# Kernel optimization log

Measured on AMD Instinct MI355X. Metric: run time of the kernel, lower is better.

The kernel has to match this reference:

```python
import jax, jax.numpy as jnp
import numpy as np

TEMP1 = 4.0  # local_temp1 default


def setup_inputs() -> dict:
    key = jax.random.key(0)
    k1, k2 = jax.random.split(key)
    query = jax.random.normal(k1, (256, 768, 96), dtype=jnp.float32)
    context = jax.random.normal(k2, (256, 768, 19, 19), dtype=jnp.float32)
    return {"query": query, "context": context}


def reference(query, context):
    # query: [B, ndf, Q]; context: [B, ndf, ih, iw]
    B, ndf, Q = query.shape
    ih, iw = context.shape[2], context.shape[3]
    S = ih * iw
    ctx = context.reshape(B, ndf, S)            # [B, ndf, S]
    # attn = contextT @ query -> [B, S, Q]
    attn = jnp.einsum('bds,bdq->bsq', ctx, query)
    # softmax over query dim
    attn = jax.nn.softmax(attn, axis=-1)
    # transpose to [B, Q, S], temperature scale, softmax over source dim
    attn = jnp.swapaxes(attn, 1, 2) * TEMP1
    attn = jax.nn.softmax(attn, axis=-1)        # [B, Q, S]
    # weightedContext = context @ attn^T -> [B, ndf, Q]
    weighted_context = jnp.einsum('bds,bqs->bdq', ctx, attn)
    attn_map = attn.reshape(B, Q, ih, iw)
    return weighted_context, attn_map
```

## Files before the change

### kernel.cpp

```cpp
#include <hip/hip_runtime.h>

#define NB 256
#define NDF 768
#define NQ 96
#define NS 361
#define LDT 40
#define LDP 392
#define WSROW 368
#define CSROW 368
#define WS_LOG_BYTES ((size_t)NB * NQ * WSROW * 2)
#define WS_CTX_BYTES ((size_t)NB * NDF * CSROW * 2)
#define WS_FULL_BYTES (WS_LOG_BYTES + WS_CTX_BYTES)

typedef short bf16x8_t __attribute__((ext_vector_type(8)));
typedef float f32x4_t __attribute__((ext_vector_type(4)));
typedef float f32x4u_t __attribute__((ext_vector_type(4), aligned(4)));
typedef float f32x2u_t __attribute__((ext_vector_type(2), aligned(4)));
typedef unsigned int u32x2_t __attribute__((ext_vector_type(2)));
typedef unsigned int u32x4_t __attribute__((ext_vector_type(4)));

__device__ __forceinline__ unsigned pack_hi(unsigned b_, unsigned a_) {
    return __builtin_amdgcn_perm(b_, a_, 0x07060302u);
}
__device__ __forceinline__ unsigned short f2bf(float x) {
    unsigned u = __float_as_uint(x);
    u += 0x7FFFu + ((u >> 16) & 1u);
    return (unsigned short)(u >> 16);
}
__device__ __forceinline__ float bf2f(unsigned short h) {
    return __uint_as_float(((unsigned)h) << 16);
}

__device__ __forceinline__ void block_sync_lds() {
    __builtin_amdgcn_sched_barrier(0);
    asm volatile("s_waitcnt lgkmcnt(0)" ::: "memory");
    __builtin_amdgcn_sched_barrier(0);
    __builtin_amdgcn_s_barrier();
    __builtin_amdgcn_sched_barrier(0);
}

template<int MODE>
__global__ __launch_bounds__(384, 3) void k1_gemm1_softmaxq(
    const float* __restrict__ Qg, const float* __restrict__ Cg,
    unsigned short* __restrict__ WsLog, unsigned* __restrict__ WsCtxD,
    float* __restrict__ AoutF)
{
    __shared__ unsigned short sQhi[NQ * LDT];
    __shared__ unsigned short sQlo[NQ * LDT];
    __shared__ unsigned short sShi[192 * LDT];
    __shared__ unsigned short sSlo[192 * LDT];

    const int b = blockIdx.x >> 1;
    const int h = blockIdx.x & 1;
    const int tid = threadIdx.x;
    const int wv = tid >> 6;
    const int lane = tid & 63;
    const int ll = lane & 15;
    const int lg = lane >> 4;
    const int s0 = 192 * h;
    const int qq  = tid % NQ;
    const int kqQ = tid / NQ;
    const int sp  = tid % 96;
    const int kqb = tid / 96;
    const int sA0 = s0 + 2 * sp;
    const bool ok0 = (sA0 < NS);
    const bool ok1 = (sA0 + 1 < NS);
    const int wsCol = 96 * h + sp;
    const bool wok = (MODE == 2) && (wsCol < 184);

    const float* __restrict__ qg = Qg + (size_t)b * NDF * NQ;
    const float* __restrict__ cg = Cg + (size_t)b * NDF * NS;
    unsigned* __restrict__ wscd = (MODE == 2) ? (WsCtxD + (size_t)b * NDF * 184) : nullptr;

    f32x4_t acc[6][2];
#pragma unroll
    for (int i = 0; i < 6; ++i)
#pragma unroll
        for (int j = 0; j < 2; ++j) acc[i][j] = (f32x4_t)0.0f;

    float RQa[8], RQb[8];
    float RCa[16], RCb[16];

#define LOADQ(K0, R) { \
    const float* p = qg + ((K0) + 4 * kqQ) * NQ + qq; \
    R[0] = p[0]; R[1] = p[NQ]; R[2] = p[2 * NQ]; R[3] = p[3 * NQ]; \
    const float* p2 = p + 16 * NQ; \
    R[4] = p2[0]; R[5] = p2[NQ]; R[6] = p2[2 * NQ]; R[7] = p2[3 * NQ]; }

#define LOADC(K0, R) { \
    _Pragma("unroll") \
    for (int k2 = 0; k2 < 2; ++k2) { \
        const float* p = cg + ((K0) + 4 * (kqb + 4 * k2)) * NS; \
        _Pragma("unroll") \
        for (int j = 0; j < 4; ++j) { \
            const float* pj = p + j * NS + sA0; \
            f32x2u_t v; \
            if (ok1) { v = *(const f32x2u_t*)pj; } \
            else { v[0] = ok0 ? pj[0] : 0.0f; v[1] = 0.0f; } \
            R[(k2 * 4 + j) * 2 + 0] = v[0]; \
            R[(k2 * 4 + j) * 2 + 1] = v[1]; } } }

#define STOREQ(R) { \
    _Pragma("unroll") \
    for (int t = 0; t < 2; ++t) { \
        unsigned u0 = __float_as_uint(R[4*t+0]), u1 = __float_as_uint(R[4*t+1]); \
        unsigned u2 = __float_as_uint(R[4*t+2]), u3 = __float_as_uint(R[4*t+3]); \
        float l0 = R[4*t+0] - __uint_as_float(u0 & 0xFFFF0000u); \
        float l1 = R[4*t+1] - __uint_as_float(u1 & 0xFFFF0000u); \
        float l2 = R[4*t+2] - __uint_as_float(u2 & 0xFFFF0000u); \
        float l3 = R[4*t+3] - __uint_as_float(u3 & 0xFFFF0000u); \
        u32x2_t hi, lo; \
        hi[0] = pack_hi(u1, u0); hi[1] = pack_hi(u3, u2); \
        lo[0] = pack_hi(__float_as_uint(l1), __float_as_uint(l0)); \
        lo[1] = pack_hi(__float_as_uint(l3), __float_as_uint(l2)); \
        int off = qq * LDT + 4 * (kqQ + 4 * t); \
        *(u32x2_t*)&sQhi[off] = hi; \
        *(u32x2_t*)&sQlo[off] = lo; } }

#define STOREC(K0, R) { \
    _Pragma("unroll") \
    for (int k2 = 0; k2 < 2; ++k2) { \
        const int kq = kqb + 4 * k2; \
        unsigned u[4][2]; float l[4][2]; \
        _Pragma("unroll") \
        for (int j = 0; j < 4; ++j) { \
            _Pragma("unroll") \
            for (int s1 = 0; s1 < 2; ++s1) { \
                float x = R[(k2 * 4 + j) * 2 + s1]; \
                u[j][s1] = __float_as_uint(x); \
                l[j][s1] = x - __uint_as_float(u[j][s1] & 0xFFFF0000u); } } \
        _Pragma("unroll") \
        for (int s1 = 0; s1 < 2; ++s1) { \
            u32x2_t hi, lo; \
            hi[0] = pack_hi(u[1][s1], u[0][s1]); \
            hi[1] = pack_hi(u[3][s1], u[2][s1]); \
            lo[0] = pack_hi(__float_as_uint(l[1][s1]), __float_as_uint(l[0][s1])); \
            lo[1] = pack_hi(__float_as_uint(l[3][s1]), __float_as_uint(l[2][s1])); \
            int off = (2 * sp + s1) * LDT + 4 * kq; \
            *(u32x2_t*)&sShi[off] = hi; \
            *(u32x2_t*)&sSlo[off] = lo; } \
        if (wok) { \
            _Pragma("unroll") \
            for (int j = 0; j < 4; ++j) \
                wscd[(size_t)((K0) + 4 * kq + j) * 184 + wsCol] = pack_hi(u[j][1], u[j][0]); } } }

#define FRAGMFMA() { \
    bf16x8_t Bhi[2], Blo[2]; \
    _Pragma("unroll") \
    for (int nt = 0; nt < 2; ++nt) { \
        int row = 32 * wv + 16 * nt + ll; \
        Bhi[nt] = *(const bf16x8_t*)&sShi[row * LDT + 8 * lg]; \
        Blo[nt] = *(const bf16x8_t*)&sSlo[row * LDT + 8 * lg]; } \
    _Pragma("unroll") \
    for (int mt = 0; mt < 6; ++mt) { \
        int row = 16 * mt + ll; \
        bf16x8_t Ahi = *(const bf16x8_t*)&sQhi[row * LDT + 8 * lg]; \
        bf16x8_t Alo = *(const bf16x8_t*)&sQlo[row * LDT + 8 * lg]; \
        _Pragma("unroll") \
        for (int nt = 0; nt < 2; ++nt) { \
            acc[mt][nt] = __builtin_amdgcn_mfma_f32_16x16x32_bf16(Ahi, Bhi[nt], acc[mt][nt], 0, 0, 0); \
            acc[mt][nt] = __builtin_amdgcn_mfma_f32_16x16x32_bf16(Ahi, Blo[nt], acc[mt][nt], 0, 0, 0); \
            acc[mt][nt] = __builtin_amdgcn_mfma_f32_16x16x32_bf16(Alo, Bhi[nt], acc[mt][nt], 0, 0, 0); } } }

    LOADQ(0, RQa); LOADC(0, RCa);
    for (int k0 = 0; k0 < NDF; k0 += 64) {
        STOREQ(RQa); STOREC(k0, RCa);
        block_sync_lds();
        if (k0 + 32 < NDF) { LOADQ(k0 + 32, RQb); LOADC(k0 + 32, RCb); }
        __builtin_amdgcn_sched_barrier(0);
        FRAGMFMA();
        block_sync_lds();
        STOREQ(RQb); STOREC(k0 + 32, RCb);
        block_sync_lds();
        if (k0 + 64 < NDF) { LOADQ(k0 + 64, RQa); LOADC(k0 + 64, RCa); }
        __builtin_amdgcn_sched_barrier(0);
        FRAGMFMA();
        block_sync_lds();
    }
#undef LOADQ
#undef LOADC
#undef STOREQ
#undef STOREC
#undef FRAGMFMA

#pragma unroll
    for (int nt = 0; nt < 2; ++nt) {
        float m = -3.0e38f;
#pragma unroll
        for (int mt = 0; mt < 6; ++mt)
#pragma unroll
            for (int r = 0; r < 4; ++r) m = fmaxf(m, acc[mt][nt][r]);
        m = fmaxf(m, __shfl_xor(m, 16));
        m = fmaxf(m, __shfl_xor(m, 32));
        float sum = 0.0f;
#pragma unroll
        for (int mt = 0; mt < 6; ++mt)
#pragma unroll
            for (int r = 0; r < 4; ++r) {
                float e = __expf(acc[mt][nt][r] - m);
                acc[mt][nt][r] = e;
                sum += e;
            }
        sum += __shfl_xor(sum, 16);
        sum += __shfl_xor(sum, 32);
        float inv = 4.0f / sum;
#pragma unroll
        for (int mt = 0; mt < 6; ++mt)
#pragma unroll
            for (int r = 0; r < 4; ++r) acc[mt][nt][r] *= inv;
    }

    if constexpr (MODE >= 1) {
        unsigned short* wr = WsLog + (size_t)b * NQ * WSROW;
#pragma unroll
        for (int mt = 0; mt < 6; ++mt)
#pragma unroll
            for (int nt = 0; nt < 2; ++nt)
#pragma unroll
                for (int r = 0; r < 4; ++r) {
                    int q = 16 * mt + 4 * lg + r;
                    int s = s0 + 32 * wv + 16 * nt + ll;
                    if (s < NS) wr[q * WSROW + s] = f2bf(acc[mt][nt][r]);
                }
    } else {
        float* aout = AoutF + (size_t)b * NQ * NS;
#pragma unroll
        for (int mt = 0; mt < 6; ++mt)
#pragma unroll
            for (int nt = 0; nt < 2; ++nt)
#pragma unroll
                for (int r = 0; r < 4; ++r) {
                    int q = 16 * mt + 4 * lg + r;
                    int s = s0 + 32 * wv + 16 * nt + ll;
                    if (s < NS) aout[(size_t)q * NS + s] = acc[mt][nt][r];
                }
    }
}

__global__ __launch_bounds__(256) void k15_softmaxs(float* __restrict__ Aout)
{
    const int b = blockIdx.x;
    const int q = blockIdx.y * 4 + (threadIdx.x >> 6);
    const int lane = threadIdx.x & 63;
    float* __restrict__ row = Aout + ((size_t)b * NQ + q) * NS;
    const int c0 = 6 * lane;

    float v[6];
#pragma unroll
    for (int i = 0; i < 6; ++i) v[i] = (c0 + i < NS) ? row[c0 + i] : -INFINITY;
    float m = v[0];
#pragma unroll
    for (int i = 1; i < 6; ++i) m = fmaxf(m, v[i]);
#pragma unroll
    for (int o = 1; o < 64; o <<= 1) m = fmaxf(m, __shfl_xor(m, o));
    float e[6], sum = 0.0f;
#pragma unroll
    for (int i = 0; i < 6; ++i) { e[i] = __expf(v[i] - m); sum += e[i]; }
#pragma unroll
    for (int o = 1; o < 64; o <<= 1) sum += __shfl_xor(sum, o);
    float inv = 1.0f / sum;
#pragma unroll
    for (int i = 0; i < 6; ++i) if (c0 + i < NS) row[c0 + i] = e[i] * inv;
}

template<int MODE>
__global__ __launch_bounds__(512, 4) void k2_gemm2(
    const float* __restrict__ Cg, const unsigned short* __restrict__ WsLog,
    const unsigned short* __restrict__ WsCtx,
    const float* __restrict__ AttnF, float* __restrict__ Wout, float* __restrict__ AoutF)
{
    extern __shared__ char smem2[];
    unsigned short* sP = (unsigned short*)smem2;
    unsigned* sPd = (unsigned*)smem2;
    float* sMax = (float*)(smem2 + NQ * LDP * 2);
    float* sInv = sMax + NQ;

    const int b = blockIdx.x >> 2;
    const int quarter = blockIdx.x & 3;
    const int tid = threadIdx.x;
    const int wv = tid >> 6;
    const int lane = tid & 63;
    const int ll = lane & 15;
    const int lg = lane >> 4;

    if constexpr (MODE >= 1) {
        const unsigned* __restrict__ wsd = (const unsigned*)(WsLog + (size_t)b * NQ * WSROW);
        for (int i = tid; i < NQ * 184; i += 512) {
            int r = i / 184, c = i - r * 184;
            sPd[r * 196 + c] = wsd[i];
        }
        for (int i = tid; i < NQ * 12; i += 512) {
            int r = i / 12, c = i - r * 12;
            sPd[r * 196 + 184 + c] = 0;
        }
        __syncthreads();

        const int l32 = tid & 31;
        const int rbase = tid >> 5;
#pragma unroll
        for (int pass = 0; pass < 6; ++pass) {
            int row = pass * 16 + rbase;
            float m = -3.0e38f;
#pragma unroll
            for (int j = 0; j < 6; ++j) {
                int dw = l32 + 32 * j;
                if (dw < 184) {
                    unsigned u = sPd[row * 196 + dw];
                    float v0 = bf2f((unsigned short)(u & 0xFFFFu));
                    float v1 = bf2f((unsigned short)(u >> 16));
                    if (2 * dw < NS) m = fmaxf(m, v0);
                    if (2 * dw + 1 < NS) m = fmaxf(m, v1);
                }
            }
#pragma unroll
            for (int o = 1; o < 32; o <<= 1) m = fmaxf(m, __shfl_xor(m, o));
            if (l32 == 0) sMax[row] = m;
        }
        __syncthreads();
#pragma unroll
        for (int pass = 0; pass < 6; ++pass) {
            int row = pass * 16 + rbase;
            float m = sMax[row];
            float sum = 0.0f;
#pragma unroll
            for (int j = 0; j < 6; ++j) {
                int dw = l32 + 32 * j;
                if (dw < 184) {
                    unsigned u = sPd[row * 196 + dw];
                    float v0 = bf2f((unsigned short)(u & 0xFFFFu));
                    float v1 = bf2f((unsigned short)(u >> 16));
                    float e0 = (2 * dw < NS) ? __expf(v0 - m) : 0.0f;
                    float e1 = (2 * dw + 1 < NS) ? __expf(v1 - m) : 0.0f;
                    sum += e0 + e1;
                    sPd[row * 196 + dw] = ((unsigned)f2bf(e1) << 16) | (unsigned)f2bf(e0);
                }
            }
#pragma unroll
            for (int o = 1; o < 32; o <<= 1) sum += __shfl_xor(sum, o);
            if (l32 == 0) sInv[row] = sum;
        }
        __syncthreads();
        if (tid < NQ) sInv[tid] = 1.0f / sInv[tid];
        __syncthreads();
        if (quarter == 0) {
            float* aout = AoutF + (size_t)b * NQ * NS;
            for (int i = tid; i < NQ * NS; i += 512) {
                int q = i / NS, s = i - q * NS;
                aout[i] = bf2f(sP[q * LDP + s]) * sInv[q];
            }
        }
    } else {
        const float* __restrict__ attn = AttnF + (size_t)b * NQ * NS;
        for (int i = tid; i < NQ * 181; i += 512) {
            int row = i / 181, p = i - row * 181;
            float x0 = attn[row * NS + 2 * p];
            float x1 = (p < 180) ? attn[row * NS + 2 * p + 1] : 0.0f;
            sPd[row * 196 + p] = pack_hi(__float_as_uint(x1), __float_as_uint(x0));
        }
        for (int i = tid; i < NQ * 15; i += 512) {
            int row = i / 15, p = i - row * 15;
            sPd[row * 196 + 181 + p] = 0;
        }
        __syncthreads();
    }

    f32x4_t acc[3][3];
#pragma unroll
    for (int i = 0; i < 3; ++i)
#pragma unroll
        for (int j = 0; j < 3; ++j) acc[i][j] = (f32x4_t)0.0f;

    const int dw = wv >> 1, qw = wv & 1;
    const float* __restrict__ cq = Cg + (size_t)b * NDF * NS + (size_t)(quarter * 192) * NS;
    const unsigned short* __restrict__ cb =
        (MODE == 2) ? (WsCtx + ((size_t)b * NDF + quarter * 192) * CSROW) : nullptr;

#pragma unroll
    for (int c = 0; c < 12; ++c) {
        bf16x8_t Bf[3];
#pragma unroll
        for (int nt = 0; nt < 3; ++nt) {
            int row = 16 * (3 * qw + nt) + ll;
            Bf[nt] = *(const bf16x8_t*)&sP[row * LDP + 32 * c + 8 * lg];
        }
#pragma unroll
        for (int i = 0; i < 3; ++i) {
            int d = 16 * (3 * dw + i) + ll;
            bf16x8_t Af;
            if constexpr (MODE == 2) {
                if (c < 11 || lg < 2) {
                    Af = *(const bf16x8_t*)&cb[(size_t)d * CSROW + 32 * c + 8 * lg];
                } else {
                    Af = (bf16x8_t)0;
                }
            } else {
                const float* ap = cq + (size_t)d * NS + 32 * c + 8 * lg;
                u32x4_t u;
                if (c < 11) {
                    f32x4u_t a0 = *(const f32x4u_t*)ap;
                    f32x4u_t a1 = *(const f32x4u_t*)(ap + 4);
                    u[0] = pack_hi(__float_as_uint(a0[1]), __float_as_uint(a0[0]));
                    u[1] = pack_hi(__float_as_uint(a0[3]), __float_as_uint(a0[2]));
                    u[2] = pack_hi(__float_as_uint(a1[1]), __float_as_uint(a1[0]));
                    u[3] = pack_hi(__float_as_uint(a1[3]), __float_as_uint(a1[2]));
                } else {
                    float t[8];
#pragma unroll
                    for (int e = 0; e < 8; ++e) {
                        int s = 352 + 8 * lg + e;
                        t[e] = (s < NS) ? ap[e] : 0.0f;
                    }
                    u[0] = pack_hi(__float_as_uint(t[1]), __float_as_uint(t[0]));
                    u[1] = pack_hi(__float_as_uint(t[3]), __float_as_uint(t[2]));
                    u[2] = pack_hi(__float_as_uint(t[5]), __float_as_uint(t[4]));
                    u[3] = pack_hi(__float_as_uint(t[7]), __float_as_uint(t[6]));
                }
                Af = __builtin_bit_cast(bf16x8_t, u);
            }
#pragma unroll
            for (int nt = 0; nt < 3; ++nt)
                acc[i][nt] = __builtin_amdgcn_mfma_f32_16x16x32_bf16(Af, Bf[nt], acc[i][nt], 0, 0, 0);
        }
    }

    float* wout = Wout + (size_t)b * NDF * NQ;
    float invq[3];
#pragma unroll
    for (int nt = 0; nt < 3; ++nt) {
        if constexpr (MODE >= 1) invq[nt] = sInv[16 * (3 * qw + nt) + ll];
        else invq[nt] = 1.0f;
    }
#pragma unroll
    for (int i = 0; i < 3; ++i)
#pragma unroll
        for (int nt = 0; nt < 3; ++nt)
#pragma unroll
            for (int r = 0; r < 4; ++r) {
                int d = quarter * 192 + 16 * (3 * dw + i) + 4 * lg + r;
                int q = 16 * (3 * qw + nt) + ll;
                wout[(size_t)d * NQ + q] = acc[i][nt][r] * invq[nt];
            }
}

extern "C" void kernel_launch(void* const* d_in, const int* in_sizes, int n_in,
                              void* d_out, int out_size, void* d_ws, size_t ws_size,
                              hipStream_t stream) {
    const float* Qg = (const float*)d_in[0];
    const float* Cg = (const float*)d_in[1];
    float* Wout = (float*)d_out;
    float* Aout = Wout + (size_t)NB * NDF * NQ;

    const int smem2 = NQ * LDP * 2 + NQ * 8;

    if (ws_size >= WS_FULL_BYTES) {
        unsigned short* wsLog = (unsigned short*)d_ws;
        unsigned* wsCtxD = (unsigned*)((char*)d_ws + WS_LOG_BYTES);
        k1_gemm1_softmaxq<2><<<dim3(NB * 2), dim3(384), 0, stream>>>(Qg, Cg, wsLog, wsCtxD, nullptr);
        (void)hipFuncSetAttribute((const void*)k2_gemm2<2>,
                                  hipFuncAttributeMaxDynamicSharedMemorySize, smem2);
        k2_gemm2<2><<<dim3(NB * 4), dim3(512), smem2, stream>>>(
            Cg, wsLog, (const unsigned short*)wsCtxD, nullptr, Wout, Aout);
    } else if (ws_size >= WS_LOG_BYTES) {
        unsigned short* wsLog = (unsigned short*)d_ws;
        k1_gemm1_softmaxq<1><<<dim3(NB * 2), dim3(384), 0, stream>>>(Qg, Cg, wsLog, nullptr, nullptr);
        (void)hipFuncSetAttribute((const void*)k2_gemm2<1>,
                                  hipFuncAttributeMaxDynamicSharedMemorySize, smem2);
        k2_gemm2<1><<<dim3(NB * 4), dim3(512), smem2, stream>>>(
            Cg, wsLog, nullptr, nullptr, Wout, Aout);
    } else {
        k1_gemm1_softmaxq<0><<<dim3(NB * 2), dim3(384), 0, stream>>>(Qg, Cg, nullptr, nullptr, Aout);
        k15_softmaxs<<<dim3(NB, 24), dim3(256), 0, stream>>>(Aout);
        (void)hipFuncSetAttribute((const void*)k2_gemm2<0>,
                                  hipFuncAttributeMaxDynamicSharedMemorySize, smem2);
        k2_gemm2<0><<<dim3(NB * 4), dim3(512), smem2, stream>>>(
            Cg, nullptr, nullptr, Aout, Wout, Aout);
    }
}
```

Measured before the change: 223.2 us.

## Split first GEMM into four source-column tiles per batch for higher occupancy

```diff
diff --git a/kernel.cpp b/kernel.cpp
--- a/kernel.cpp
+++ b/kernel.cpp
@@ -40,137 +40,101 @@
 }
 
 template<int MODE>
-__global__ __launch_bounds__(384, 3) void k1_gemm1_softmaxq(
+__global__ __launch_bounds__(384, 6) void k1_gemm1_softmaxq(
     const float* __restrict__ Qg, const float* __restrict__ Cg,
     unsigned short* __restrict__ WsLog, unsigned* __restrict__ WsCtxD,
     float* __restrict__ AoutF)
 {
     __shared__ unsigned short sQhi[NQ * LDT];
     __shared__ unsigned short sQlo[NQ * LDT];
-    __shared__ unsigned short sShi[192 * LDT];
-    __shared__ unsigned short sSlo[192 * LDT];
-
-    const int b = blockIdx.x >> 1;
-    const int h = blockIdx.x & 1;
+    __shared__ unsigned short sShi[NQ * LDT];
+    __shared__ unsigned short sSlo[NQ * LDT];
+
+    const int b = blockIdx.x >> 2;
+    const int h = blockIdx.x & 3;
     const int tid = threadIdx.x;
     const int wv = tid >> 6;
     const int lane = tid & 63;
     const int ll = lane & 15;
     const int lg = lane >> 4;
-    const int s0 = 192 * h;
-    const int qq  = tid % NQ;
-    const int kqQ = tid / NQ;
-    const int sp  = tid % 96;
-    const int kqb = tid / 96;
-    const int sA0 = s0 + 2 * sp;
+    const int s0 = 96 * h;
+    const int qp  = tid % 48;
+    const int kq8 = tid / 48;
+    const int sA0 = s0 + 2 * qp;
     const bool ok0 = (sA0 < NS);
     const bool ok1 = (sA0 + 1 < NS);
-    const int wsCol = 96 * h + sp;
+    const int wsCol = 48 * h + qp;
     const bool wok = (MODE == 2) && (wsCol < 184);
 
     const float* __restrict__ qg = Qg + (size_t)b * NDF * NQ;
     const float* __restrict__ cg = Cg + (size_t)b * NDF * NS;
     unsigned* __restrict__ wscd = (MODE == 2) ? (WsCtxD + (size_t)b * NDF * 184) : nullptr;
 
-    f32x4_t acc[6][2];
-#pragma unroll
-    for (int i = 0; i < 6; ++i)
-#pragma unroll
-        for (int j = 0; j < 2; ++j) acc[i][j] = (f32x4_t)0.0f;
-
-    float RQa[8], RQb[8];
-    float RCa[16], RCb[16];
+    f32x4_t acc[6];
+#pragma unroll
+    for (int i = 0; i < 6; ++i) acc[i] = (f32x4_t)0.0f;
+
+    float RQa[8], RQb[8], RCa[8], RCb[8];
 
 #define LOADQ(K0, R) { \
-    const float* p = qg + ((K0) + 4 * kqQ) * NQ + qq; \
-    R[0] = p[0]; R[1] = p[NQ]; R[2] = p[2 * NQ]; R[3] = p[3 * NQ]; \
-    const float* p2 = p + 16 * NQ; \
-    R[4] = p2[0]; R[5] = p2[NQ]; R[6] = p2[2 * NQ]; R[7] = p2[3 * NQ]; }
+    _Pragma("unroll") \
+    for (int j = 0; j < 4; ++j) { \
+        f32x2u_t v = *(const f32x2u_t*)(qg + ((K0) + 4 * kq8 + j) * NQ + 2 * qp); \
+        R[2*j+0] = v[0]; R[2*j+1] = v[1]; } }
 
 #define LOADC(K0, R) { \
     _Pragma("unroll") \
-    for (int k2 = 0; k2 < 2; ++k2) { \
-        const float* p = cg + ((K0) + 4 * (kqb + 4 * k2)) * NS; \
-        _Pragma("unroll") \
-        for (int j = 0; j < 4; ++j) { \
-            const float* pj = p + j * NS + sA0; \
-            f32x2u_t v; \
-            if (ok1) { v = *(const f32x2u_t*)pj; } \
-            else { v[0] = ok0 ? pj[0] : 0.0f; v[1] = 0.0f; } \
-            R[(k2 * 4 + j) * 2 + 0] = v[0]; \
-            R[(k2 * 4 + j) * 2 + 1] = v[1]; } } }
-
-#define STOREQ(R) { \
+    for (int j = 0; j < 4; ++j) { \
+        const float* pj = cg + ((K0) + 4 * kq8 + j) * NS + sA0; \
+        f32x2u_t v; \
+        if (ok1) { v = *(const f32x2u_t*)pj; } \
+        else { v[0] = ok0 ? pj[0] : 0.0f; v[1] = 0.0f; } \
+        R[2*j+0] = v[0]; R[2*j+1] = v[1]; } }
+
+#define STORE2(R, DSTH, DSTL) { \
     _Pragma("unroll") \
-    for (int t = 0; t < 2; ++t) { \
-        unsigned u0 = __float_as_uint(R[4*t+0]), u1 = __float_as_uint(R[4*t+1]); \
-        unsigned u2 = __float_as_uint(R[4*t+2]), u3 = __float_as_uint(R[4*t+3]); \
-        float l0 = R[4*t+0] - __uint_as_float(u0 & 0xFFFF0000u); \
-        float l1 = R[4*t+1] - __uint_as_float(u1 & 0xFFFF0000u); \
-        float l2 = R[4*t+2] - __uint_as_float(u2 & 0xFFFF0000u); \
-        float l3 = R[4*t+3] - __uint_as_float(u3 & 0xFFFF0000u); \
+    for (int s1 = 0; s1 < 2; ++s1) { \
+        unsigned u0 = __float_as_uint(R[0+s1]), u1 = __float_as_uint(R[2+s1]); \
+        unsigned u2 = __float_as_uint(R[4+s1]), u3 = __float_as_uint(R[6+s1]); \
+        float l0 = R[0+s1] - __uint_as_float(u0 & 0xFFFF0000u); \
+        float l1 = R[2+s1] - __uint_as_float(u1 & 0xFFFF0000u); \
+        float l2 = R[4+s1] - __uint_as_float(u2 & 0xFFFF0000u); \
+        float l3 = R[6+s1] - __uint_as_float(u3 & 0xFFFF0000u); \
         u32x2_t hi, lo; \
         hi[0] = pack_hi(u1, u0); hi[1] = pack_hi(u3, u2); \
         lo[0] = pack_hi(__float_as_uint(l1), __float_as_uint(l0)); \
         lo[1] = pack_hi(__float_as_uint(l3), __float_as_uint(l2)); \
-        int off = qq * LDT + 4 * (kqQ + 4 * t); \
-        *(u32x2_t*)&sQhi[off] = hi; \
-        *(u32x2_t*)&sQlo[off] = lo; } }
-
-#define STOREC(K0, R) { \
-    _Pragma("unroll") \
-    for (int k2 = 0; k2 < 2; ++k2) { \
-        const int kq = kqb + 4 * k2; \
-        unsigned u[4][2]; float l[4][2]; \
+        int off = (2 * qp + s1) * LDT + 4 * kq8; \
+        *(u32x2_t*)&(DSTH)[off] = hi; \
+        *(u32x2_t*)&(DSTL)[off] = lo; } }
+
+#define RELAYC(K0, R) { \
+    if (wok) { \
         _Pragma("unroll") \
-        for (int j = 0; j < 4; ++j) { \
-            _Pragma("unroll") \
-            for (int s1 = 0; s1 < 2; ++s1) { \
-                float x = R[(k2 * 4 + j) * 2 + s1]; \
-                u[j][s1] = __float_as_uint(x); \
-                l[j][s1] = x - __uint_as_float(u[j][s1] & 0xFFFF0000u); } } \
-        _Pragma("unroll") \
-        for (int s1 = 0; s1 < 2; ++s1) { \
-            u32x2_t hi, lo; \
-            hi[0] = pack_hi(u[1][s1], u[0][s1]); \
-            hi[1] = pack_hi(u[3][s1], u[2][s1]); \
-            lo[0] = pack_hi(__float_as_uint(l[1][s1]), __float_as_uint(l[0][s1])); \
-            lo[1] = pack_hi(__float_as_uint(l[3][s1]), __float_as_uint(l[2][s1])); \
-            int off = (2 * sp + s1) * LDT + 4 * kq; \
-            *(u32x2_t*)&sShi[off] = hi; \
-            *(u32x2_t*)&sSlo[off] = lo; } \
-        if (wok) { \
-            _Pragma("unroll") \
-            for (int j = 0; j < 4; ++j) \
-                wscd[(size_t)((K0) + 4 * kq + j) * 184 + wsCol] = pack_hi(u[j][1], u[j][0]); } } }
+        for (int j = 0; j < 4; ++j) \
+            wscd[(size_t)((K0) + 4 * kq8 + j) * 184 + wsCol] = \
+                pack_hi(__float_as_uint(R[2*j+1]), __float_as_uint(R[2*j+0])); } }
 
 #define FRAGMFMA() { \
-    bf16x8_t Bhi[2], Blo[2]; \
-    _Pragma("unroll") \
-    for (int nt = 0; nt < 2; ++nt) { \
-        int row = 32 * wv + 16 * nt + ll; \
-        Bhi[nt] = *(const bf16x8_t*)&sShi[row * LDT + 8 * lg]; \
-        Blo[nt] = *(const bf16x8_t*)&sSlo[row * LDT + 8 * lg]; } \
+    bf16x8_t Bhi = *(const bf16x8_t*)&sShi[(16 * wv + ll) * LDT + 8 * lg]; \
+    bf16x8_t Blo = *(const bf16x8_t*)&sSlo[(16 * wv + ll) * LDT + 8 * lg]; \
     _Pragma("unroll") \
     for (int mt = 0; mt < 6; ++mt) { \
-        int row = 16 * mt + ll; \
-        bf16x8_t Ahi = *(const bf16x8_t*)&sQhi[row * LDT + 8 * lg]; \
-        bf16x8_t Alo = *(const bf16x8_t*)&sQlo[row * LDT + 8 * lg]; \
-        _Pragma("unroll") \
-        for (int nt = 0; nt < 2; ++nt) { \
-            acc[mt][nt] = __builtin_amdgcn_mfma_f32_16x16x32_bf16(Ahi, Bhi[nt], acc[mt][nt], 0, 0, 0); \
-            acc[mt][nt] = __builtin_amdgcn_mfma_f32_16x16x32_bf16(Ahi, Blo[nt], acc[mt][nt], 0, 0, 0); \
-            acc[mt][nt] = __builtin_amdgcn_mfma_f32_16x16x32_bf16(Alo, Bhi[nt], acc[mt][nt], 0, 0, 0); } } }
+        bf16x8_t Ahi = *(const bf16x8_t*)&sQhi[(16 * mt + ll) * LDT + 8 * lg]; \
+        bf16x8_t Alo = *(const bf16x8_t*)&sQlo[(16 * mt + ll) * LDT + 8 * lg]; \
+        acc[mt] = __builtin_amdgcn_mfma_f32_16x16x32_bf16(Ahi, Bhi, acc[mt], 0, 0, 0); \
+        acc[mt] = __builtin_amdgcn_mfma_f32_16x16x32_bf16(Ahi, Blo, acc[mt], 0, 0, 0); \
+        acc[mt] = __builtin_amdgcn_mfma_f32_16x16x32_bf16(Alo, Bhi, acc[mt], 0, 0, 0); } }
 
     LOADQ(0, RQa); LOADC(0, RCa);
     for (int k0 = 0; k0 < NDF; k0 += 64) {
-        STOREQ(RQa); STOREC(k0, RCa);
+        STORE2(RQa, sQhi, sQlo); STORE2(RCa, sShi, sSlo); RELAYC(k0, RCa);
         block_sync_lds();
         if (k0 + 32 < NDF) { LOADQ(k0 + 32, RQb); LOADC(k0 + 32, RCb); }
         __builtin_amdgcn_sched_barrier(0);
         FRAGMFMA();
         block_sync_lds();
-        STOREQ(RQb); STOREC(k0 + 32, RCb);
+        STORE2(RQb, sQhi, sQlo); STORE2(RCb, sShi, sSlo); RELAYC(k0 + 32, RCb);
         block_sync_lds();
         if (k0 + 64 < NDF) { LOADQ(k0 + 64, RQa); LOADC(k0 + 64, RCa); }
         __builtin_amdgcn_sched_barrier(0);
@@ -179,17 +143,16 @@
     }
 #undef LOADQ
 #undef LOADC
-#undef STOREQ
-#undef STOREC
+#undef STORE2
+#undef RELAYC
 #undef FRAGMFMA
 
-#pragma unroll
-    for (int nt = 0; nt < 2; ++nt) {
+    {
         float m = -3.0e38f;
 #pragma unroll
         for (int mt = 0; mt < 6; ++mt)
 #pragma unroll
-            for (int r = 0; r < 4; ++r) m = fmaxf(m, acc[mt][nt][r]);
+            for (int r = 0; r < 4; ++r) m = fmaxf(m, acc[mt][r]);
         m = fmaxf(m, __shfl_xor(m, 16));
         m = fmaxf(m, __shfl_xor(m, 32));
         float sum = 0.0f;
@@ -197,8 +160,8 @@
         for (int mt = 0; mt < 6; ++mt)
 #pragma unroll
             for (int r = 0; r < 4; ++r) {
-                float e = __expf(acc[mt][nt][r] - m);
-                acc[mt][nt][r] = e;
+                float e = __expf(acc[mt][r] - m);
+                acc[mt][r] = e;
                 sum += e;
             }
         sum += __shfl_xor(sum, 16);
@@ -207,33 +170,32 @@
 #pragma unroll
         for (int mt = 0; mt < 6; ++mt)
 #pragma unroll
-            for (int r = 0; r < 4; ++r) acc[mt][nt][r] *= inv;
-    }
-
+            for (int r = 0; r < 4; ++r) acc[mt][r] *= inv;
+    }
+
+    const int sOut = s0 + 16 * wv + ll;
     if constexpr (MODE >= 1) {
         unsigned short* wr = WsLog + (size_t)b * NQ * WSROW;
-#pragma unroll
-        for (int mt = 0; mt < 6; ++mt)
-#pragma unroll
-            for (int nt = 0; nt < 2; ++nt)
+        if (sOut < NS) {
+#pragma unroll
+            for (int mt = 0; mt < 6; ++mt)
 #pragma unroll
                 for (int r = 0; r < 4; ++r) {
                     int q = 16 * mt + 4 * lg + r;
-                    int s = s0 + 32 * wv + 16 * nt + ll;
-                    if (s < NS) wr[q * WSROW + s] = f2bf(acc[mt][nt][r]);
-                }
+                    wr[q * WSROW + sOut] = f2bf(acc[mt][r]);
+                }
+        }
     } else {
         float* aout = AoutF + (size_t)b * NQ * NS;
-#pragma unroll
-        for (int mt = 0; mt < 6; ++mt)
-#pragma unroll
-            for (int nt = 0; nt < 2; ++nt)
+        if (sOut < NS) {
+#pragma unroll
+            for (int mt = 0; mt < 6; ++mt)
 #pragma unroll
                 for (int r = 0; r < 4; ++r) {
                     int q = 16 * mt + 4 * lg + r;
-                    int s = s0 + 32 * wv + 16 * nt + ll;
-                    if (s < NS) aout[(size_t)q * NS + s] = acc[mt][nt][r];
-                }
+                    aout[(size_t)q * NS + sOut] = acc[mt][r];
+                }
+        }
     }
 }
 
@@ -455,20 +417,20 @@
     if (ws_size >= WS_FULL_BYTES) {
         unsigned short* wsLog = (unsigned short*)d_ws;
         unsigned* wsCtxD = (unsigned*)((char*)d_ws + WS_LOG_BYTES);
-        k1_gemm1_softmaxq<2><<<dim3(NB * 2), dim3(384), 0, stream>>>(Qg, Cg, wsLog, wsCtxD, nullptr);
+        k1_gemm1_softmaxq<2><<<dim3(NB * 4), dim3(384), 0, stream>>>(Qg, Cg, wsLog, wsCtxD, nullptr);
         (void)hipFuncSetAttribute((const void*)k2_gemm2<2>,
                                   hipFuncAttributeMaxDynamicSharedMemorySize, smem2);
         k2_gemm2<2><<<dim3(NB * 4), dim3(512), smem2, stream>>>(
             Cg, wsLog, (const unsigned short*)wsCtxD, nullptr, Wout, Aout);
     } else if (ws_size >= WS_LOG_BYTES) {
         unsigned short* wsLog = (unsigned short*)d_ws;
-        k1_gemm1_softmaxq<1><<<dim3(NB * 2), dim3(384), 0, stream>>>(Qg, Cg, wsLog, nullptr, nullptr);
+        k1_gemm1_softmaxq<1><<<dim3(NB * 4), dim3(384), 0, stream>>>(Qg, Cg, wsLog, nullptr, nullptr);
         (void)hipFuncSetAttribute((const void*)k2_gemm2<1>,
                                   hipFuncAttributeMaxDynamicSharedMemorySize, smem2);
         k2_gemm2<1><<<dim3(NB * 4), dim3(512), smem2, stream>>>(
             Cg, wsLog, nullptr, nullptr, Wout, Aout);
     } else {
-        k1_gemm1_softmaxq<0><<<dim3(NB * 2), dim3(384), 0, stream>>>(Qg, Cg, nullptr, nullptr, Aout);
+        k1_gemm1_softmaxq<0><<<dim3(NB * 4), dim3(384), 0, stream>>>(Qg, Cg, nullptr, nullptr, Aout);
         k15_softmaxs<<<dim3(NB, 24), dim3(256), 0, stream>>>(Aout);
         (void)hipFuncSetAttribute((const void*)k2_gemm2<0>,
                                   hipFuncAttributeMaxDynamicSharedMemorySize, smem2);
```

New measurement: 285.7 us. +28.0%, slower.
